# Kernel tuning notes

Hardware: AMD Instinct MI355X
Metric: run time of the kernel (lower is better)

## Reference

```python
import jax, jax.numpy as jnp
import numpy as np

N, S, C, E = 32768, 32768, 1024, 16384   # nodes, subgraph-node entries, clusters (=B*P), coarsen edges
F, D, B, P, NC = 64, 64, 16, 64, 10      # feat dim, hidden, graphs, patches per graph, classes


def setup_inputs():
    key = jax.random.key(0)
    ks = list(jax.random.split(key, 24))
    p = lambda k, shp: jax.random.normal(k, shp, dtype=jnp.float32) * 0.05
    z = lambda n: jnp.zeros((n,), jnp.float32)
    return {
        "x": jax.random.normal(ks[0], (N, F), dtype=jnp.float32),
        "subgraphs_nodes_mapper": jax.random.randint(ks[1], (S,), 0, N, dtype=jnp.int32),
        "subgraphs_batch": jnp.sort(jax.random.randint(ks[2], (S,), 0, C, dtype=jnp.int32)),
        "subgraphs_batch_row": jax.random.randint(ks[3], (E,), 0, C, dtype=jnp.int32),
        "subgraphs_batch_col": jax.random.randint(ks[4], (E,), 0, C, dtype=jnp.int32),
        "coarsen_edge_attr": jax.random.uniform(ks[5], (E,), dtype=jnp.float32),
        "W_in1": p(ks[6], (F, D)), "b_in1": z(D),
        "W_in2": p(ks[7], (D, D)), "b_in2": z(D),
        "W_pre1": p(ks[8], (D, D)), "b_pre1": z(D),
        "W_pre2": p(ks[9], (D, D)), "b_pre2": z(D),
        "W_post1": p(ks[10], (D, D)), "b_post1": z(D),
        "W_post2": p(ks[11], (D, D)), "b_post2": z(D),
        "W_K": p(ks[12], (D, D)), "b_K": z(D),
        "W_V": p(ks[13], (D, D)), "b_V": z(D),
        "alpha_beta": jax.random.normal(ks[14], (2,), dtype=jnp.float32),
        "W_c1": p(ks[15], (D, D // 2)), "b_c1": z(D // 2),
        "W_c2": p(ks[16], (D // 2, NC)), "b_c2": z(NC),
    }


def reference(x, subgraphs_nodes_mapper, subgraphs_batch, subgraphs_batch_row,
              subgraphs_batch_col, coarsen_edge_attr,
              W_in1, b_in1, W_in2, b_in2, W_pre1, b_pre1, W_pre2, b_pre2,
              W_post1, b_post1, W_post2, b_post2, W_K, b_K, W_V, b_V,
              alpha_beta, W_c1, b_c1, W_c2, b_c2):
    seg_sum = lambda v, idx: jax.ops.segment_sum(v, idx, num_segments=C)
    # input transform MLP (use_gnn=False path)
    h = jax.nn.relu(x @ W_in1 + b_in1)
    h = jax.nn.relu(h @ W_in2 + b_in2)
    sx = h[subgraphs_nodes_mapper]                        # [S, D] irregular gather
    b = subgraphs_batch
    row, col = subgraphs_batch_row, subgraphs_batch_col
    # bincount-based symmetric degree normalization of coarsened edge weights
    deg = seg_sum(coarsen_edge_attr, row)                 # [C]
    dinv = jnp.where(deg > 0, deg ** -0.5, 0.0)
    ea = dinv[row] * coarsen_edge_attr * dinv[col]        # [E]
    # Q path: pre-deepset -> scatter sum -> post-deepset
    Q = jax.nn.relu(sx @ W_pre1 + b_pre1) @ W_pre2 + b_pre2
    Qs = seg_sum(Q, b)
    Qs = jax.nn.relu(Qs @ W_post1 + b_post1) @ W_post2 + b_post2  # [C, D]
    # K / V paths
    K = sx @ W_K + b_K                                    # [S, D]
    cnt = jnp.maximum(seg_sum(jnp.ones((S,), sx.dtype), b), 1.0)
    Ks = seg_sum(K, b) / cnt[:, None]                     # scatter-mean [C, D]
    V = sx @ W_V + b_V                                    # [S, D]
    # relu kernelization
    Qk, Kk, Ksk = jax.nn.relu(Qs), jax.nn.relu(K), jax.nn.relu(Ks)
    ab = jax.nn.softmax(alpha_beta)
    sa, sb = ab[0] ** -0.5, ab[1] ** -0.5
    ck = jnp.concatenate([sa * Ksk[b], sb * Kk], axis=-1)   # [S, 2D]
    cq = jnp.concatenate([sa * Qk, sb * Qk], axis=-1)       # [C, 2D] (diffQ=False)
    ck_s = seg_sum(ck, b)                                   # [C, 2D]
    M = ck[:, :, None] * V[:, None, :]                      # [S, 2D, D] per-entry outer product
    Ms = seg_sum(M, b)                                      # [C, 2D, D]
    # Double_Level_MessageProp / KeyProp on coarsened graph: out[c] = sum_e ea_e * x[row_e] at col_e
    Ms = seg_sum(ea[:, None, None] * Ms[row], col)
    ck_s = seg_sum(ea[:, None] * ck_s[row], col)
    H = jnp.einsum('ci,cij->cj', cq, Ms)                    # [C, D]
    den = jnp.sum(cq * ck_s, axis=-1, keepdims=True) + 1e-6
    out = H / den                                           # [C, D]
    g = out.reshape(B, P, D).mean(axis=1)                   # mean readout over patches
    logits = jax.nn.relu(g @ W_c1 + b_c1) @ W_c2 + b_c2     # [B, NC]
    return logits
```

## Files before the change

kernel.cpp:

```cpp
#include <hip/hip_runtime.h>
#include <math.h>

constexpr int NN = 32768;
constexpr int SS = 32768;
constexpr int CC = 1024;
constexpr int EE = 16384;
constexpr int BB = 16;
constexpr int PP = 64;
constexpr int NC = 10;

__device__ __forceinline__ float rdlane(float v, int l) {
    return __int_as_float(__builtin_amdgcn_readlane(__float_as_int(v), l));
}

#define TS 68

__device__ __forceinline__ void gemm64(const float* A, const float* W,
                                       const float* __restrict__ bias,
                                       int r0, int c0, float acc[4][4])
{
#pragma unroll
    for (int dc = 0; dc < 4; ++dc) {
        float bv = bias[c0 + dc];
        acc[0][dc] = bv; acc[1][dc] = bv; acc[2][dc] = bv; acc[3][dc] = bv;
    }
#pragma unroll 16
    for (int k = 0; k < 64; ++k) {
        float4 av = *(const float4*)(A + k * TS + r0);
        float4 wv = *(const float4*)(W + k * TS + c0);
        acc[0][0] = fmaf(av.x, wv.x, acc[0][0]); acc[0][1] = fmaf(av.x, wv.y, acc[0][1]);
        acc[0][2] = fmaf(av.x, wv.z, acc[0][2]); acc[0][3] = fmaf(av.x, wv.w, acc[0][3]);
        acc[1][0] = fmaf(av.y, wv.x, acc[1][0]); acc[1][1] = fmaf(av.y, wv.y, acc[1][1]);
        acc[1][2] = fmaf(av.y, wv.z, acc[1][2]); acc[1][3] = fmaf(av.y, wv.w, acc[1][3]);
        acc[2][0] = fmaf(av.z, wv.x, acc[2][0]); acc[2][1] = fmaf(av.z, wv.y, acc[2][1]);
        acc[2][2] = fmaf(av.z, wv.z, acc[2][2]); acc[2][3] = fmaf(av.z, wv.w, acc[2][3]);
        acc[3][0] = fmaf(av.w, wv.x, acc[3][0]); acc[3][1] = fmaf(av.w, wv.y, acc[3][1]);
        acc[3][2] = fmaf(av.w, wv.z, acc[3][2]); acc[3][3] = fmaf(av.w, wv.w, acc[3][3]);
    }
}

__device__ __forceinline__ void gemm64x2(const float* A, const float* Wa, const float* Wb,
                                         const float* __restrict__ bias1,
                                         const float* __restrict__ bias2,
                                         int r0, int c0, float acc1[4][4], float acc2[4][4])
{
#pragma unroll
    for (int dc = 0; dc < 4; ++dc) {
        float bv1 = bias1[c0 + dc], bv2 = bias2[c0 + dc];
#pragma unroll
        for (int dr = 0; dr < 4; ++dr) { acc1[dr][dc] = bv1; acc2[dr][dc] = bv2; }
    }
#pragma unroll 8
    for (int k = 0; k < 64; ++k) {
        float4 av = *(const float4*)(A + k * TS + r0);
        float4 w1 = *(const float4*)(Wa + k * TS + c0);
        float4 w2 = *(const float4*)(Wb + k * TS + c0);
        float ar[4] = {av.x, av.y, av.z, av.w};
        float u1[4] = {w1.x, w1.y, w1.z, w1.w};
        float u2[4] = {w2.x, w2.y, w2.z, w2.w};
#pragma unroll
        for (int dr = 0; dr < 4; ++dr)
#pragma unroll
            for (int dc = 0; dc < 4; ++dc) {
                acc1[dr][dc] = fmaf(ar[dr], u1[dc], acc1[dr][dc]);
                acc2[dr][dc] = fmaf(ar[dr], u2[dc], acc2[dr][dc]);
            }
    }
}

__device__ __forceinline__ void writeW(float* dst, int tid,
                                       float4 a, float4 b, float4 c, float4 d)
{
    int colq = (tid & 15) * 4;
    int rb = tid >> 4;
    *(float4*)(dst + (rb     ) * TS + colq) = a;
    *(float4*)(dst + (rb + 16) * TS + colq) = b;
    *(float4*)(dst + (rb + 32) * TS + colq) = c;
    *(float4*)(dst + (rb + 48) * TS + colq) = d;
}

__device__ __forceinline__ void writeXT(float* dst, int tid,
                                        float4 a, float4 b, float4 c, float4 d)
{
    int rb = (tid * 4) & 63;
    int cb = tid >> 4;
    dst[(rb + 0) * TS + cb     ] = a.x;
    dst[(rb + 1) * TS + cb     ] = a.y;
    dst[(rb + 2) * TS + cb     ] = a.z;
    dst[(rb + 3) * TS + cb     ] = a.w;
    dst[(rb + 0) * TS + cb + 16] = b.x;
    dst[(rb + 1) * TS + cb + 16] = b.y;
    dst[(rb + 2) * TS + cb + 16] = b.z;
    dst[(rb + 3) * TS + cb + 16] = b.w;
    dst[(rb + 0) * TS + cb + 32] = c.x;
    dst[(rb + 1) * TS + cb + 32] = c.y;
    dst[(rb + 2) * TS + cb + 32] = c.z;
    dst[(rb + 3) * TS + cb + 32] = c.w;
    dst[(rb + 0) * TS + cb + 48] = d.x;
    dst[(rb + 1) * TS + cb + 48] = d.y;
    dst[(rb + 2) * TS + cb + 48] = d.z;
    dst[(rb + 3) * TS + cb + 48] = d.w;
}

__device__ __forceinline__ void outT_relu(float* dst, int r0, int c0, float acc[4][4])
{
#pragma unroll
    for (int dc = 0; dc < 4; ++dc) {
        *(float4*)(dst + (c0 + dc) * TS + r0) =
            make_float4(fmaxf(acc[0][dc], 0.f), fmaxf(acc[1][dc], 0.f),
                        fmaxf(acc[2][dc], 0.f), fmaxf(acc[3][dc], 0.f));
    }
}

__device__ __forceinline__ void outG2(float* __restrict__ dst, size_t rowbase, int ld,
                                      int off, int r0, int c0, float acc[4][4], bool dorelu)
{
#pragma unroll
    for (int dr = 0; dr < 4; ++dr) {
        float4 v = make_float4(acc[dr][0], acc[dr][1], acc[dr][2], acc[dr][3]);
        if (dorelu) {
            v.x = fmaxf(v.x, 0.f); v.y = fmaxf(v.y, 0.f);
            v.z = fmaxf(v.z, 0.f); v.w = fmaxf(v.w, 0.f);
        }
        *(float4*)(dst + (rowbase + r0 + dr) * ld + off + c0) = v;
    }
}

__global__ __launch_bounds__(256, 3) void k_node(
    const float* __restrict__ x,
    const int* __restrict__ row, const float* __restrict__ attr,
    const int* __restrict__ batch,
    const float* __restrict__ W1, const float* __restrict__ b1,
    const float* __restrict__ W2, const float* __restrict__ b2,
    const float* __restrict__ Wp1, const float* __restrict__ bp1,
    const float* __restrict__ WK, const float* __restrict__ bK,
    const float* __restrict__ WV, const float* __restrict__ bV,
    float* __restrict__ u, float* __restrict__ KV,
    float* __restrict__ deg, int* __restrict__ segoff, float* __restrict__ zbase)
{
    __shared__ __align__(16) float bufA[64 * TS];
    __shared__ __align__(16) float bufB[64 * TS];
    __shared__ __align__(16) float w0[64 * TS];
    __shared__ float ldeg[16];
    int tid = threadIdx.x;
    int b = blockIdx.x;
    if (tid < 33) {
        int i = b * 33 + tid;
        if (i < 16640) ((float4*)zbase)[i] = make_float4(0.f, 0.f, 0.f, 0.f);
    }
    if (b < 64) {
        if (tid < 16) ldeg[tid] = 0.f;
        __syncthreads();
        int lo = b * 16;
#pragma unroll 4
        for (int i = 0; i < 64; ++i) {
            int e = i * 256 + tid;
            int r = row[e];
            unsigned d = (unsigned)(r - lo);
            if (d < 16u) atomicAdd(&ldeg[d], attr[e]);
        }
        __syncthreads();
        if (tid < 16) deg[lo + tid] = ldeg[tid];
    } else if (b < 192) {
        int t = (b - 64) * 256 + tid;
        int cur = batch[t];
        int prev = (t == 0) ? -1 : batch[t - 1];
        for (int c = prev + 1; c <= cur; ++c) segoff[c] = t;
        if (t == SS - 1)
            for (int c = cur + 1; c <= CC; ++c) segoff[c] = SS;
    }
    int tx = tid & 15, ty = tid >> 4;
    int r0 = ty * 4, c0 = tx * 4;
    size_t rowbase = (size_t)b * 64;
    const float* xb = x + rowbase * 64;
    float4 a0 = ((const float4*)W1)[tid];
    float4 a1 = ((const float4*)W1)[tid + 256];
    float4 a2 = ((const float4*)W1)[tid + 512];
    float4 a3 = ((const float4*)W1)[tid + 768];
    float4 x0 = ((const float4*)xb)[tid];
    float4 x1 = ((const float4*)xb)[tid + 256];
    float4 x2 = ((const float4*)xb)[tid + 512];
    float4 x3 = ((const float4*)xb)[tid + 768];
    writeW(w0, tid, a0, a1, a2, a3);
    writeXT(bufA, tid, x0, x1, x2, x3);
    __syncthreads();
    float acc[4][4], acc2[4][4];
    a0 = ((const float4*)W2)[tid];
    a1 = ((const float4*)W2)[tid + 256];
    a2 = ((const float4*)W2)[tid + 512];
    a3 = ((const float4*)W2)[tid + 768];
    gemm64(bufA, w0, b1, r0, c0, acc);
    outT_relu(bufB, r0, c0, acc);
    __syncthreads();
    writeW(w0, tid, a0, a1, a2, a3);
    __syncthreads();
    a0 = ((const float4*)Wp1)[tid];
    a1 = ((const float4*)Wp1)[tid + 256];
    a2 = ((const float4*)Wp1)[tid + 512];
    a3 = ((const float4*)Wp1)[tid + 768];
    float4 k0 = ((const float4*)WK)[tid];
    float4 k1 = ((const float4*)WK)[tid + 256];
    float4 k2 = ((const float4*)WK)[tid + 512];
    float4 k3 = ((const float4*)WK)[tid + 768];
    gemm64(bufB, w0, b2, r0, c0, acc);
    outT_relu(bufA, r0, c0, acc);
    __syncthreads();
    writeW(w0, tid, a0, a1, a2, a3);
    writeW(bufB, tid, k0, k1, k2, k3);
    __syncthreads();
    a0 = ((const float4*)WV)[tid];
    a1 = ((const float4*)WV)[tid + 256];
    a2 = ((const float4*)WV)[tid + 512];
    a3 = ((const float4*)WV)[tid + 768];
    gemm64x2(bufA, w0, bufB, bp1, bK, r0, c0, acc, acc2);
    outG2(u, rowbase, 64, 0, r0, c0, acc, true);
    outG2(KV, rowbase, 128, 0, r0, c0, acc2, false);
    __syncthreads();
    writeW(w0, tid, a0, a1, a2, a3);
    __syncthreads();
    gemm64(bufA, w0, bV, r0, c0, acc);
    outG2(KV, rowbase, 128, 64, r0, c0, acc, false);
}

__global__ __launch_bounds__(256, 4) void k_qk(
    const float* __restrict__ u, const int* __restrict__ mapper,
    const int* __restrict__ segoff,
    const float* __restrict__ Wp2, const float* __restrict__ bp2,
    const float* __restrict__ Wpo1, const float* __restrict__ bpo1,
    const float* __restrict__ Wpo2, const float* __restrict__ bpo2,
    float* __restrict__ Qk)
{
    __shared__ float accs[4][64];
    int c = blockIdx.x;
    int tid = threadIdx.x, j = tid & 63, g = tid >> 6;
    int s0 = segoff[c], s1 = segoff[c + 1];
    float L = (float)(s1 - s0);
    if (tid < 64) {
        accs[0][tid] = 0.f;
        accs[1][tid] = L * bp2[tid];
        accs[2][tid] = bpo1[tid];
        accs[3][tid] = bpo2[tid];
    }
    __syncthreads();
    float us = 0.f;
    for (int s = s0 + g; s < s1; s += 4) us += u[(size_t)mapper[s] * 64 + j];
    atomicAdd(&accs[0][j], us);
    __syncthreads();
    float usv = accs[0][j];
    float p = 0.f;
#pragma unroll
    for (int t = 0; t < 16; ++t) {
        int i = g * 16 + t;
        p = fmaf(rdlane(usv, i), Wp2[i * 64 + j], p);
    }
    atomicAdd(&accs[1][j], p);
    __syncthreads();
    float qs = accs[1][j];
    p = 0.f;
#pragma unroll
    for (int t = 0; t < 16; ++t) {
        int i = g * 16 + t;
        p = fmaf(rdlane(qs, i), Wpo1[i * 64 + j], p);
    }
    atomicAdd(&accs[2][j], p);
    __syncthreads();
    float tv = fmaxf(accs[2][j], 0.f);
    p = 0.f;
#pragma unroll
    for (int t = 0; t < 16; ++t) {
        int i = g * 16 + t;
        p = fmaf(rdlane(tv, i), Wpo2[i * 64 + j], p);
    }
    atomicAdd(&accs[3][j], p);
    __syncthreads();
    if (g == 0) Qk[c * 64 + j] = fmaxf(accs[3][j], 0.f);
}

#define KSTR 72
#define MSTR 68

__global__ __launch_bounds__(256, 4) void k_msbedge(
    const float* __restrict__ KV, const int* __restrict__ mapper,
    const int* __restrict__ segoff, const float* __restrict__ Qk,
    const int* __restrict__ row, const int* __restrict__ col,
    const float* __restrict__ attr, const float* __restrict__ deg,
    const float* __restrict__ ab,
    float* __restrict__ H, float* __restrict__ den)
{
    __shared__ __align__(16) float Kr[32 * KSTR];
    __shared__ __align__(16) float Vb[32 * KSTR];
    __shared__ __align__(16) float msb[64 * MSTR];
    __shared__ int map_lds[32];
    __shared__ float sums[192];
    __shared__ float dvec[64];
    __shared__ int eids[128];
    __shared__ int ecol[144];
    __shared__ float ewt[144];
    __shared__ int ecnt;
    int c = blockIdx.x;
    int tid = threadIdx.x, j = tid & 63, g = tid >> 6;
    int tx = tid & 15, ty = tid >> 4;
    int r0 = ty * 4, c0 = tx * 4;
    if (tid == 0) ecnt = 0;
    if (tid < 192) sums[tid] = 0.f;
    __syncthreads();
#pragma unroll 4
    for (int i = 0; i < 64; ++i) {
        int e = i * 256 + tid;
        if (row[e] == c) {
            int p = atomicAdd(&ecnt, 1);
            if (p < 128) eids[p] = e;
        }
    }
    __syncthreads();
    int ne = min(ecnt, 128);
    if (ne == 0) return;
    int s0 = segoff[c], s1 = segoff[c + 1];
    float acc[4][4];
#pragma unroll
    for (int a = 0; a < 4; ++a)
#pragma unroll
        for (int bq = 0; bq < 4; ++bq) acc[a][bq] = 0.f;
    float ks = 0.f, krs = 0.f, vs = 0.f;
    for (int sb = s0; sb < s1; sb += 32) {
        int clen = min(32, s1 - sb);
        __syncthreads();
        if (tid < clen) map_lds[tid] = mapper[sb + tid];
        __syncthreads();
        for (int p = tid; p < clen * 32; p += 256) {
            int e = p >> 5, q = p & 31;
            int m = map_lds[e];
            float4 v = *(const float4*)(KV + (size_t)m * 128 + q * 4);
            float* dst = (q < 16) ? &Kr[e * KSTR + q * 4] : &Vb[e * KSTR + (q - 16) * 4];
            *(float4*)dst = v;
        }
        __syncthreads();
#pragma unroll 4
        for (int s = 0; s < clen; ++s) {
            float4 a4 = *(const float4*)(&Kr[s * KSTR + r0]);
            float4 b4 = *(const float4*)(&Vb[s * KSTR + c0]);
            float ar0 = fmaxf(a4.x, 0.f), ar1 = fmaxf(a4.y, 0.f);
            float ar2 = fmaxf(a4.z, 0.f), ar3 = fmaxf(a4.w, 0.f);
            acc[0][0] = fmaf(ar0, b4.x, acc[0][0]); acc[0][1] = fmaf(ar0, b4.y, acc[0][1]);
            acc[0][2] = fmaf(ar0, b4.z, acc[0][2]); acc[0][3] = fmaf(ar0, b4.w, acc[0][3]);
            acc[1][0] = fmaf(ar1, b4.x, acc[1][0]); acc[1][1] = fmaf(ar1, b4.y, acc[1][1]);
            acc[1][2] = fmaf(ar1, b4.z, acc[1][2]); acc[1][3] = fmaf(ar1, b4.w, acc[1][3]);
            acc[2][0] = fmaf(ar2, b4.x, acc[2][0]); acc[2][1] = fmaf(ar2, b4.y, acc[2][1]);
            acc[2][2] = fmaf(ar2, b4.z, acc[2][2]); acc[2][3] = fmaf(ar2, b4.w, acc[2][3]);
            acc[3][0] = fmaf(ar3, b4.x, acc[3][0]); acc[3][1] = fmaf(ar3, b4.y, acc[3][1]);
            acc[3][2] = fmaf(ar3, b4.z, acc[3][2]); acc[3][3] = fmaf(ar3, b4.w, acc[3][3]);
        }
        for (int s = g; s < clen; s += 4) {
            float kv = Kr[s * KSTR + j];
            ks += kv;
            krs += fmaxf(kv, 0.f);
            vs += Vb[s * KSTR + j];
        }
    }
    atomicAdd(&sums[j], ks);
    atomicAdd(&sums[64 + j], krs);
    atomicAdd(&sums[128 + j], vs);
    __syncthreads();
    int L = s1 - s0;
    float Lr = (float)L;
    float invLm = 1.f / (float)(L > 0 ? L : 1);
    float a0 = ab[0], a1 = ab[1];
    float sa2 = 1.f + expf(a1 - a0);
    float sb2 = 1.f + expf(a0 - a1);
    float dr = deg[c];
    float dinvr = dr > 0.f ? 1.f / sqrtf(dr) : 0.f;
    if (tid < 64) {
        float kskv = fmaxf(sums[tid] * invLm, 0.f);
        dvec[tid] = sa2 * Lr * kskv + sb2 * sums[64 + tid];
    }
    float4 vsl4 = *(const float4*)(&sums[128 + c0]);
#pragma unroll
    for (int a = 0; a < 4; ++a) {
        float kska = fmaxf(sums[r0 + a] * invLm, 0.f) * sa2;
        *(float4*)(&msb[(r0 + a) * MSTR + c0]) =
            make_float4(fmaf(kska, vsl4.x, sb2 * acc[a][0]),
                        fmaf(kska, vsl4.y, sb2 * acc[a][1]),
                        fmaf(kska, vsl4.z, sb2 * acc[a][2]),
                        fmaf(kska, vsl4.w, sb2 * acc[a][3]));
    }
    int nr = (ne + 15) & ~15;
    if (tid < ne) {
        int e = eids[tid];
        int cd = col[e];
        float dc = deg[cd];
        float dinvc = dc > 0.f ? 1.f / sqrtf(dc) : 0.f;
        ecol[tid] = cd;
        ewt[tid] = dinvr * attr[e] * dinvc;
    }
    for (int p = ne + tid; p < nr; p += 256) { ecol[p] = c; ewt[p] = 0.f; }
    __syncthreads();
    float dvreg = dvec[j];
    for (int m0 = g * 4; m0 < nr; m0 += 16) {
        int cd0 = ecol[m0 + 0], cd1 = ecol[m0 + 1];
        int cd2 = ecol[m0 + 2], cd3 = ecol[m0 + 3];
        float wt0 = ewt[m0 + 0], wt1 = ewt[m0 + 1];
        float wt2 = ewt[m0 + 2], wt3 = ewt[m0 + 3];
        float q0 = Qk[(size_t)cd0 * 64 + j];
        float q1 = Qk[(size_t)cd1 * 64 + j];
        float q2 = Qk[(size_t)cd2 * 64 + j];
        float q3 = Qk[(size_t)cd3 * 64 + j];
        float o0 = 0.f, o1 = 0.f, o2 = 0.f, o3 = 0.f;
#pragma unroll
        for (int i = 0; i < 64; ++i) {
            float mv = msb[i * MSTR + j];
            o0 = fmaf(rdlane(q0, i), mv, o0);
            o1 = fmaf(rdlane(q1, i), mv, o1);
            o2 = fmaf(rdlane(q2, i), mv, o2);
            o3 = fmaf(rdlane(q3, i), mv, o3);
        }
        float p0 = q0 * dvreg, p1 = q1 * dvreg, p2 = q2 * dvreg, p3 = q3 * dvreg;
#pragma unroll
        for (int o = 32; o > 0; o >>= 1) {
            p0 += __shfl_xor(p0, o);
            p1 += __shfl_xor(p1, o);
            p2 += __shfl_xor(p2, o);
            p3 += __shfl_xor(p3, o);
        }
        atomicAdd(&H[(size_t)cd0 * 64 + j], wt0 * o0);
        atomicAdd(&H[(size_t)cd1 * 64 + j], wt1 * o1);
        atomicAdd(&H[(size_t)cd2 * 64 + j], wt2 * o2);
        atomicAdd(&H[(size_t)cd3 * 64 + j], wt3 * o3);
        if (j == 0) {
            atomicAdd(&den[cd0], wt0 * p0);
            atomicAdd(&den[cd1], wt1 * p1);
            atomicAdd(&den[cd2], wt2 * p2);
            atomicAdd(&den[cd3], wt3 * p3);
        }
    }
}

__global__ __launch_bounds__(64) void k_final(
    const float* __restrict__ H, const float* __restrict__ den,
    const float* __restrict__ Wc1, const float* __restrict__ bc1,
    const float* __restrict__ Wc2, const float* __restrict__ bc2,
    float* __restrict__ out)
{
    int bg = blockIdx.x;
    int j = threadIdx.x;
    float acc = 0.f;
    for (int p = 0; p < PP; ++p) {
        int c = bg * PP + p;
        acc += H[c * 64 + j] / (den[c] + 1e-6f);
    }
    float g = acc * (1.f / (float)PP);
    int m = j & 31;
    float a1 = bc1[m];
#pragma unroll
    for (int i = 0; i < 64; ++i) a1 = fmaf(rdlane(g, i), Wc1[i * 32 + m], a1);
    float c1 = fmaxf(a1, 0.f);
    int n = (j < NC) ? j : 0;
    float a2 = bc2[n];
#pragma unroll
    for (int i = 0; i < 32; ++i) a2 = fmaf(rdlane(c1, i), Wc2[i * NC + n], a2);
    if (j < NC) out[bg * NC + j] = a2;
}

extern "C" void kernel_launch(void* const* d_in, const int* in_sizes, int n_in,
                              void* d_out, int out_size, void* d_ws, size_t ws_size,
                              hipStream_t stream)
{
    const float* x      = (const float*)d_in[0];
    const int*   mapper = (const int*)d_in[1];
    const int*   batch  = (const int*)d_in[2];
    const int*   row    = (const int*)d_in[3];
    const int*   col    = (const int*)d_in[4];
    const float* attr   = (const float*)d_in[5];
    const float* W_in1  = (const float*)d_in[6];
    const float* b_in1  = (const float*)d_in[7];
    const float* W_in2  = (const float*)d_in[8];
    const float* b_in2  = (const float*)d_in[9];
    const float* W_pre1 = (const float*)d_in[10];
    const float* b_pre1 = (const float*)d_in[11];
    const float* W_pre2 = (const float*)d_in[12];
    const float* b_pre2 = (const float*)d_in[13];
    const float* W_post1= (const float*)d_in[14];
    const float* b_post1= (const float*)d_in[15];
    const float* W_post2= (const float*)d_in[16];
    const float* b_post2= (const float*)d_in[17];
    const float* W_K    = (const float*)d_in[18];
    const float* b_K    = (const float*)d_in[19];
    const float* W_V    = (const float*)d_in[20];
    const float* b_V    = (const float*)d_in[21];
    const float* alpha_beta = (const float*)d_in[22];
    const float* W_c1   = (const float*)d_in[23];
    const float* b_c1   = (const float*)d_in[24];
    const float* W_c2   = (const float*)d_in[25];
    const float* b_c2   = (const float*)d_in[26];

    float* ws = (float*)d_ws;
    float* u     = ws;
    float* KV    = u     + (size_t)NN * 64;
    float* Qk    = KV    + (size_t)NN * 128;
    float* deg   = Qk    + (size_t)CC * 64;
    float* H     = deg   + (size_t)CC;
    float* den   = H     + (size_t)CC * 64;
    int*  segoff = (int*)(den + (size_t)CC);

    k_node<<<NN / 64, 256, 0, stream>>>(x, row, attr, batch,
                                        W_in1, b_in1, W_in2, b_in2,
                                        W_pre1, b_pre1, W_K, b_K, W_V, b_V,
                                        u, KV, deg, segoff, H);
    k_qk<<<CC, 256, 0, stream>>>(u, mapper, segoff, W_pre2, b_pre2,
                                 W_post1, b_post1, W_post2, b_post2, Qk);
    k_msbedge<<<CC, 256, 0, stream>>>(KV, mapper, segoff, Qk, row, col,
                                      attr, deg, alpha_beta, H, den);
    k_final<<<BB, 64, 0, stream>>>(H, den, W_c1, b_c1, W_c2, b_c2, (float*)d_out);
}
```

Before: 94.71 us.

## Split msbedge into half-row blocks and fuse pre1/K/V GEMMs in k_node

k_msbedge now launches two blocks per cluster, each handling half of the 64 key rows of the outer-product accumulator. This shrinks shared memory and registers per block so more blocks fit per CU (launch bounds go from 4 to 6). The cost is that each block reloads the V rows and redoes the edge scan. k_node adds a fourth shared weight buffer and computes the pre1, K and V projections in one three-way GEMM, removing several barriers. That extra LDS lowers its occupancy target from 3 to 2 blocks.

Measured after the change: 114.3 us. 20.7% more time.

```diff
diff --git a/kernel.cpp b/kernel.cpp
--- a/kernel.cpp
+++ b/kernel.cpp
@@ -39,31 +39,37 @@
     }
 }
 
-__device__ __forceinline__ void gemm64x2(const float* A, const float* Wa, const float* Wb,
-                                         const float* __restrict__ bias1,
-                                         const float* __restrict__ bias2,
-                                         int r0, int c0, float acc1[4][4], float acc2[4][4])
+__device__ __forceinline__ void gemm64x3(const float* A, const float* Wa,
+                                         const float* Wb, const float* Wc_,
+                                         const float* __restrict__ b1_,
+                                         const float* __restrict__ b2_,
+                                         const float* __restrict__ b3_,
+                                         int r0, int c0,
+                                         float a1_[4][4], float a2_[4][4], float a3_[4][4])
 {
 #pragma unroll
     for (int dc = 0; dc < 4; ++dc) {
-        float bv1 = bias1[c0 + dc], bv2 = bias2[c0 + dc];
-#pragma unroll
-        for (int dr = 0; dr < 4; ++dr) { acc1[dr][dc] = bv1; acc2[dr][dc] = bv2; }
-    }
-#pragma unroll 8
+        float v1 = b1_[c0 + dc], v2 = b2_[c0 + dc], v3 = b3_[c0 + dc];
+#pragma unroll
+        for (int dr = 0; dr < 4; ++dr) { a1_[dr][dc] = v1; a2_[dr][dc] = v2; a3_[dr][dc] = v3; }
+    }
+#pragma unroll 4
     for (int k = 0; k < 64; ++k) {
         float4 av = *(const float4*)(A + k * TS + r0);
         float4 w1 = *(const float4*)(Wa + k * TS + c0);
         float4 w2 = *(const float4*)(Wb + k * TS + c0);
+        float4 w3 = *(const float4*)(Wc_ + k * TS + c0);
         float ar[4] = {av.x, av.y, av.z, av.w};
         float u1[4] = {w1.x, w1.y, w1.z, w1.w};
         float u2[4] = {w2.x, w2.y, w2.z, w2.w};
+        float u3[4] = {w3.x, w3.y, w3.z, w3.w};
 #pragma unroll
         for (int dr = 0; dr < 4; ++dr)
 #pragma unroll
             for (int dc = 0; dc < 4; ++dc) {
-                acc1[dr][dc] = fmaf(ar[dr], u1[dc], acc1[dr][dc]);
-                acc2[dr][dc] = fmaf(ar[dr], u2[dc], acc2[dr][dc]);
+                a1_[dr][dc] = fmaf(ar[dr], u1[dc], a1_[dr][dc]);
+                a2_[dr][dc] = fmaf(ar[dr], u2[dc], a2_[dr][dc]);
+                a3_[dr][dc] = fmaf(ar[dr], u3[dc], a3_[dr][dc]);
             }
     }
 }
@@ -126,7 +132,7 @@
     }
 }
 
-__global__ __launch_bounds__(256, 3) void k_node(
+__global__ __launch_bounds__(256, 2) void k_node(
     const float* __restrict__ x,
     const int* __restrict__ row, const float* __restrict__ attr,
     const int* __restrict__ batch,
@@ -141,6 +147,7 @@
     __shared__ __align__(16) float bufA[64 * TS];
     __shared__ __align__(16) float bufB[64 * TS];
     __shared__ __align__(16) float w0[64 * TS];
+    __shared__ __align__(16) float w1[64 * TS];
     __shared__ float ldeg[16];
     int tid = threadIdx.x;
     int b = blockIdx.x;
@@ -184,15 +191,14 @@
     writeW(w0, tid, a0, a1, a2, a3);
     writeXT(bufA, tid, x0, x1, x2, x3);
     __syncthreads();
-    float acc[4][4], acc2[4][4];
+    float acc[4][4];
     a0 = ((const float4*)W2)[tid];
     a1 = ((const float4*)W2)[tid + 256];
     a2 = ((const float4*)W2)[tid + 512];
     a3 = ((const float4*)W2)[tid + 768];
     gemm64(bufA, w0, b1, r0, c0, acc);
     outT_relu(bufB, r0, c0, acc);
-    __syncthreads();
-    writeW(w0, tid, a0, a1, a2, a3);
+    writeW(w1, tid, a0, a1, a2, a3);
     __syncthreads();
     a0 = ((const float4*)Wp1)[tid];
     a1 = ((const float4*)Wp1)[tid + 256];
@@ -202,24 +208,21 @@
     float4 k1 = ((const float4*)WK)[tid + 256];
     float4 k2 = ((const float4*)WK)[tid + 512];
     float4 k3 = ((const float4*)WK)[tid + 768];
-    gemm64(bufB, w0, b2, r0, c0, acc);
+    float4 v0 = ((const float4*)WV)[tid];
+    float4 v1 = ((const float4*)WV)[tid + 256];
+    float4 v2 = ((const float4*)WV)[tid + 512];
+    float4 v3 = ((const float4*)WV)[tid + 768];
+    gemm64(bufB, w1, b2, r0, c0, acc);
     outT_relu(bufA, r0, c0, acc);
-    __syncthreads();
     writeW(w0, tid, a0, a1, a2, a3);
-    writeW(bufB, tid, k0, k1, k2, k3);
-    __syncthreads();
-    a0 = ((const float4*)WV)[tid];
-    a1 = ((const float4*)WV)[tid + 256];
-    a2 = ((const float4*)WV)[tid + 512];
-    a3 = ((const float4*)WV)[tid + 768];
-    gemm64x2(bufA, w0, bufB, bp1, bK, r0, c0, acc, acc2);
-    outG2(u, rowbase, 64, 0, r0, c0, acc, true);
-    outG2(KV, rowbase, 128, 0, r0, c0, acc2, false);
-    __syncthreads();
-    writeW(w0, tid, a0, a1, a2, a3);
-    __syncthreads();
-    gemm64(bufA, w0, bV, r0, c0, acc);
-    outG2(KV, rowbase, 128, 64, r0, c0, acc, false);
+    writeW(w1, tid, k0, k1, k2, k3);
+    writeW(bufB, tid, v0, v1, v2, v3);
+    __syncthreads();
+    float accU[4][4], accK[4][4], accV[4][4];
+    gemm64x3(bufA, w0, w1, bufB, bp1, bK, bV, r0, c0, accU, accK, accV);
+    outG2(u, rowbase, 64, 0, r0, c0, accU, true);
+    outG2(KV, rowbase, 128, 0, r0, c0, accK, false);
+    outG2(KV, rowbase, 128, 64, r0, c0, accV, false);
 }
 
 __global__ __launch_bounds__(256, 4) void k_qk(
@@ -276,10 +279,11 @@
     if (g == 0) Qk[c * 64 + j] = fmaxf(accs[3][j], 0.f);
 }
 
-#define KSTR 72
-#define MSTR 68
-
-__global__ __launch_bounds__(256, 4) void k_msbedge(
+#define KS 36
+#define VS 72
+#define MS 68
+
+__global__ __launch_bounds__(256, 6) void k_msbedge(
     const float* __restrict__ KV, const int* __restrict__ mapper,
     const int* __restrict__ segoff, const float* __restrict__ Qk,
     const int* __restrict__ row, const int* __restrict__ col,
@@ -287,22 +291,24 @@
     const float* __restrict__ ab,
     float* __restrict__ H, float* __restrict__ den)
 {
-    __shared__ __align__(16) float Kr[32 * KSTR];
-    __shared__ __align__(16) float Vb[32 * KSTR];
-    __shared__ __align__(16) float msb[64 * MSTR];
+    __shared__ __align__(16) float pool[32 * KS + 32 * VS];
     __shared__ int map_lds[32];
-    __shared__ float sums[192];
-    __shared__ float dvec[64];
+    __shared__ float ksum[32], krsl[32], vsum[64], dvec[32];
     __shared__ int eids[128];
     __shared__ int ecol[144];
     __shared__ float ewt[144];
     __shared__ int ecnt;
-    int c = blockIdx.x;
+    float* Kr  = pool;
+    float* Vb  = pool + 32 * KS;
+    float* msb = pool;
+    int bid = blockIdx.x;
+    int c = bid >> 1, half = bid & 1;
     int tid = threadIdx.x, j = tid & 63, g = tid >> 6;
-    int tx = tid & 15, ty = tid >> 4;
-    int r0 = ty * 4, c0 = tx * 4;
+    int tr = tid >> 4, tc = tid & 15;
+    int i0 = tr * 2, c0 = tc * 4;
     if (tid == 0) ecnt = 0;
-    if (tid < 192) sums[tid] = 0.f;
+    if (tid < 32) { ksum[tid] = 0.f; krsl[tid] = 0.f; }
+    if (tid < 64) vsum[tid] = 0.f;
     __syncthreads();
 #pragma unroll 4
     for (int i = 0; i < 64; ++i) {
@@ -316,50 +322,46 @@
     int ne = min(ecnt, 128);
     if (ne == 0) return;
     int s0 = segoff[c], s1 = segoff[c + 1];
-    float acc[4][4];
-#pragma unroll
-    for (int a = 0; a < 4; ++a)
-#pragma unroll
-        for (int bq = 0; bq < 4; ++bq) acc[a][bq] = 0.f;
+    int koff = half * 32;
+    float acc[2][4] = {{0.f, 0.f, 0.f, 0.f}, {0.f, 0.f, 0.f, 0.f}};
     float ks = 0.f, krs = 0.f, vs = 0.f;
     for (int sb = s0; sb < s1; sb += 32) {
         int clen = min(32, s1 - sb);
         __syncthreads();
         if (tid < clen) map_lds[tid] = mapper[sb + tid];
         __syncthreads();
-        for (int p = tid; p < clen * 32; p += 256) {
-            int e = p >> 5, q = p & 31;
-            int m = map_lds[e];
-            float4 v = *(const float4*)(KV + (size_t)m * 128 + q * 4);
-            float* dst = (q < 16) ? &Kr[e * KSTR + q * 4] : &Vb[e * KSTR + (q - 16) * 4];
-            *(float4*)dst = v;
+        for (int p = tid; p < clen * 8; p += 256) {
+            int e = p >> 3, q = p & 7;
+            *(float4*)(&Kr[e * KS + q * 4]) =
+                *(const float4*)(KV + (size_t)map_lds[e] * 128 + koff + q * 4);
+        }
+        for (int p = tid; p < clen * 16; p += 256) {
+            int e = p >> 4, q = p & 15;
+            *(float4*)(&Vb[e * VS + q * 4]) =
+                *(const float4*)(KV + (size_t)map_lds[e] * 128 + 64 + q * 4);
         }
         __syncthreads();
 #pragma unroll 4
         for (int s = 0; s < clen; ++s) {
-            float4 a4 = *(const float4*)(&Kr[s * KSTR + r0]);
-            float4 b4 = *(const float4*)(&Vb[s * KSTR + c0]);
-            float ar0 = fmaxf(a4.x, 0.f), ar1 = fmaxf(a4.y, 0.f);
-            float ar2 = fmaxf(a4.z, 0.f), ar3 = fmaxf(a4.w, 0.f);
+            float2 a2 = *(const float2*)(&Kr[s * KS + i0]);
+            float4 b4 = *(const float4*)(&Vb[s * VS + c0]);
+            float ar0 = fmaxf(a2.x, 0.f), ar1 = fmaxf(a2.y, 0.f);
             acc[0][0] = fmaf(ar0, b4.x, acc[0][0]); acc[0][1] = fmaf(ar0, b4.y, acc[0][1]);
             acc[0][2] = fmaf(ar0, b4.z, acc[0][2]); acc[0][3] = fmaf(ar0, b4.w, acc[0][3]);
             acc[1][0] = fmaf(ar1, b4.x, acc[1][0]); acc[1][1] = fmaf(ar1, b4.y, acc[1][1]);
             acc[1][2] = fmaf(ar1, b4.z, acc[1][2]); acc[1][3] = fmaf(ar1, b4.w, acc[1][3]);
-            acc[2][0] = fmaf(ar2, b4.x, acc[2][0]); acc[2][1] = fmaf(ar2, b4.y, acc[2][1]);
-            acc[2][2] = fmaf(ar2, b4.z, acc[2][2]); acc[2][3] = fmaf(ar2, b4.w, acc[2][3]);
-            acc[3][0] = fmaf(ar3, b4.x, acc[3][0]); acc[3][1] = fmaf(ar3, b4.y, acc[3][1]);
-            acc[3][2] = fmaf(ar3, b4.z, acc[3][2]); acc[3][3] = fmaf(ar3, b4.w, acc[3][3]);
         }
         for (int s = g; s < clen; s += 4) {
-            float kv = Kr[s * KSTR + j];
-            ks += kv;
-            krs += fmaxf(kv, 0.f);
-            vs += Vb[s * KSTR + j];
-        }
-    }
-    atomicAdd(&sums[j], ks);
-    atomicAdd(&sums[64 + j], krs);
-    atomicAdd(&sums[128 + j], vs);
+            if (j < 32) {
+                float kv = Kr[s * KS + j];
+                ks += kv;
+                krs += fmaxf(kv, 0.f);
+            }
+            vs += Vb[s * VS + j];
+        }
+    }
+    if (j < 32) { atomicAdd(&ksum[j], ks); atomicAdd(&krsl[j], krs); }
+    atomicAdd(&vsum[j], vs);
     __syncthreads();
     int L = s1 - s0;
     float Lr = (float)L;
@@ -369,20 +371,23 @@
     float sb2 = 1.f + expf(a0 - a1);
     float dr = deg[c];
     float dinvr = dr > 0.f ? 1.f / sqrtf(dr) : 0.f;
-    if (tid < 64) {
-        float kskv = fmaxf(sums[tid] * invLm, 0.f);
-        dvec[tid] = sa2 * Lr * kskv + sb2 * sums[64 + tid];
-    }
-    float4 vsl4 = *(const float4*)(&sums[128 + c0]);
-#pragma unroll
-    for (int a = 0; a < 4; ++a) {
-        float kska = fmaxf(sums[r0 + a] * invLm, 0.f) * sa2;
-        *(float4*)(&msb[(r0 + a) * MSTR + c0]) =
-            make_float4(fmaf(kska, vsl4.x, sb2 * acc[a][0]),
-                        fmaf(kska, vsl4.y, sb2 * acc[a][1]),
-                        fmaf(kska, vsl4.z, sb2 * acc[a][2]),
-                        fmaf(kska, vsl4.w, sb2 * acc[a][3]));
-    }
+    {
+        float4 vsl4 = *(const float4*)(&vsum[c0]);
+        float kk0 = fmaxf(ksum[i0] * invLm, 0.f) * sa2;
+        float kk1 = fmaxf(ksum[i0 + 1] * invLm, 0.f) * sa2;
+        *(float4*)(&msb[i0 * MS + c0]) =
+            make_float4(fmaf(kk0, vsl4.x, sb2 * acc[0][0]),
+                        fmaf(kk0, vsl4.y, sb2 * acc[0][1]),
+                        fmaf(kk0, vsl4.z, sb2 * acc[0][2]),
+                        fmaf(kk0, vsl4.w, sb2 * acc[0][3]));
+        *(float4*)(&msb[(i0 + 1) * MS + c0]) =
+            make_float4(fmaf(kk1, vsl4.x, sb2 * acc[1][0]),
+                        fmaf(kk1, vsl4.y, sb2 * acc[1][1]),
+                        fmaf(kk1, vsl4.z, sb2 * acc[1][2]),
+                        fmaf(kk1, vsl4.w, sb2 * acc[1][3]));
+    }
+    if (tid < 32)
+        dvec[tid] = sa2 * Lr * fmaxf(ksum[tid] * invLm, 0.f) + sb2 * krsl[tid];
     int nr = (ne + 15) & ~15;
     if (tid < ne) {
         int e = eids[tid];
@@ -394,26 +399,27 @@
     }
     for (int p = ne + tid; p < nr; p += 256) { ecol[p] = c; ewt[p] = 0.f; }
     __syncthreads();
-    float dvreg = dvec[j];
+    float dvj = (j < 32) ? dvec[j] : 0.f;
+    int jq = half * 32 + (j & 31);
     for (int m0 = g * 4; m0 < nr; m0 += 16) {
         int cd0 = ecol[m0 + 0], cd1 = ecol[m0 + 1];
         int cd2 = ecol[m0 + 2], cd3 = ecol[m0 + 3];
         float wt0 = ewt[m0 + 0], wt1 = ewt[m0 + 1];
         float wt2 = ewt[m0 + 2], wt3 = ewt[m0 + 3];
-        float q0 = Qk[(size_t)cd0 * 64 + j];
-        float q1 = Qk[(size_t)cd1 * 64 + j];
-        float q2 = Qk[(size_t)cd2 * 64 + j];
-        float q3 = Qk[(size_t)cd3 * 64 + j];
+        float q0 = Qk[(size_t)cd0 * 64 + jq];
+        float q1 = Qk[(size_t)cd1 * 64 + jq];
+        float q2 = Qk[(size_t)cd2 * 64 + jq];
+        float q3 = Qk[(size_t)cd3 * 64 + jq];
         float o0 = 0.f, o1 = 0.f, o2 = 0.f, o3 = 0.f;
 #pragma unroll
-        for (int i = 0; i < 64; ++i) {
-            float mv = msb[i * MSTR + j];
+        for (int i = 0; i < 32; ++i) {
+            float mv = msb[i * MS + j];
             o0 = fmaf(rdlane(q0, i), mv, o0);
             o1 = fmaf(rdlane(q1, i), mv, o1);
             o2 = fmaf(rdlane(q2, i), mv, o2);
             o3 = fmaf(rdlane(q3, i), mv, o3);
         }
-        float p0 = q0 * dvreg, p1 = q1 * dvreg, p2 = q2 * dvreg, p3 = q3 * dvreg;
+        float p0 = q0 * dvj, p1 = q1 * dvj, p2 = q2 * dvj, p3 = q3 * dvj;
 #pragma unroll
         for (int o = 32; o > 0; o >>= 1) {
             p0 += __shfl_xor(p0, o);
@@ -507,7 +513,7 @@
                                         u, KV, deg, segoff, H);
     k_qk<<<CC, 256, 0, stream>>>(u, mapper, segoff, W_pre2, b_pre2,
                                  W_post1, b_post1, W_post2, b_post2, Qk);
-    k_msbedge<<<CC, 256, 0, stream>>>(KV, mapper, segoff, Qk, row, col,
-                                      attr, deg, alpha_beta, H, den);
+    k_msbedge<<<2 * CC, 256, 0, stream>>>(KV, mapper, segoff, Qk, row, col,
+                                          attr, deg, alpha_beta, H, den);
     k_final<<<BB, 64, 0, stream>>>(H, den, W_c1, b_c1, W_c2, b_c2, (float*)d_out);
 }
```

## Prebucket edges by row in node kernel and fuse Wpre1/K/V GEMMs

Applied to the files above, without the earlier changes.

Edge scanning by source row moves out of k_msbedge, where each of 1024 blocks scanned all 16384 edges. 256 extra blocks in k_node now build per-cluster edge buckets capped at 64 entries, and k_msbedge reads these precomputed lists. k_node also fuses the three final 64x64 GEMMs (pre1, K, V) into one pass using a fourth shared-memory weight buffer, which removes several barriers. The extra LDS lowers the occupancy target from 3 to 2 blocks, and the lower edge cap (64 vs 128) could drop edges if any cluster has a larger out-degree.

Result: faster. 89.94 us (-5.0%).

```diff
diff --git a/kernel.cpp b/kernel.cpp
--- a/kernel.cpp
+++ b/kernel.cpp
@@ -8,6 +8,7 @@
 constexpr int BB = 16;
 constexpr int PP = 64;
 constexpr int NC = 10;
+constexpr int ECAP = 64;
 
 __device__ __forceinline__ float rdlane(float v, int l) {
     return __int_as_float(__builtin_amdgcn_readlane(__float_as_int(v), l));
@@ -39,31 +40,37 @@
     }
 }
 
-__device__ __forceinline__ void gemm64x2(const float* A, const float* Wa, const float* Wb,
-                                         const float* __restrict__ bias1,
-                                         const float* __restrict__ bias2,
-                                         int r0, int c0, float acc1[4][4], float acc2[4][4])
+__device__ __forceinline__ void gemm64x3(const float* A, const float* Wa,
+                                         const float* Wb, const float* Wc_,
+                                         const float* __restrict__ b1_,
+                                         const float* __restrict__ b2_,
+                                         const float* __restrict__ b3_,
+                                         int r0, int c0,
+                                         float a1_[4][4], float a2_[4][4], float a3_[4][4])
 {
 #pragma unroll
     for (int dc = 0; dc < 4; ++dc) {
-        float bv1 = bias1[c0 + dc], bv2 = bias2[c0 + dc];
-#pragma unroll
-        for (int dr = 0; dr < 4; ++dr) { acc1[dr][dc] = bv1; acc2[dr][dc] = bv2; }
-    }
-#pragma unroll 8
+        float v1 = b1_[c0 + dc], v2 = b2_[c0 + dc], v3 = b3_[c0 + dc];
+#pragma unroll
+        for (int dr = 0; dr < 4; ++dr) { a1_[dr][dc] = v1; a2_[dr][dc] = v2; a3_[dr][dc] = v3; }
+    }
+#pragma unroll 4
     for (int k = 0; k < 64; ++k) {
         float4 av = *(const float4*)(A + k * TS + r0);
         float4 w1 = *(const float4*)(Wa + k * TS + c0);
         float4 w2 = *(const float4*)(Wb + k * TS + c0);
+        float4 w3 = *(const float4*)(Wc_ + k * TS + c0);
         float ar[4] = {av.x, av.y, av.z, av.w};
         float u1[4] = {w1.x, w1.y, w1.z, w1.w};
         float u2[4] = {w2.x, w2.y, w2.z, w2.w};
+        float u3[4] = {w3.x, w3.y, w3.z, w3.w};
 #pragma unroll
         for (int dr = 0; dr < 4; ++dr)
 #pragma unroll
             for (int dc = 0; dc < 4; ++dc) {
-                acc1[dr][dc] = fmaf(ar[dr], u1[dc], acc1[dr][dc]);
-                acc2[dr][dc] = fmaf(ar[dr], u2[dc], acc2[dr][dc]);
+                a1_[dr][dc] = fmaf(ar[dr], u1[dc], a1_[dr][dc]);
+                a2_[dr][dc] = fmaf(ar[dr], u2[dc], a2_[dr][dc]);
+                a3_[dr][dc] = fmaf(ar[dr], u3[dc], a3_[dr][dc]);
             }
     }
 }
@@ -126,7 +133,7 @@
     }
 }
 
-__global__ __launch_bounds__(256, 3) void k_node(
+__global__ __launch_bounds__(256, 2) void k_node(
     const float* __restrict__ x,
     const int* __restrict__ row, const float* __restrict__ attr,
     const int* __restrict__ batch,
@@ -136,12 +143,16 @@
     const float* __restrict__ WK, const float* __restrict__ bK,
     const float* __restrict__ WV, const float* __restrict__ bV,
     float* __restrict__ u, float* __restrict__ KV,
-    float* __restrict__ deg, int* __restrict__ segoff, float* __restrict__ zbase)
+    float* __restrict__ deg, int* __restrict__ segoff,
+    int* __restrict__ gcnt, int* __restrict__ ebuck,
+    float* __restrict__ zbase)
 {
     __shared__ __align__(16) float bufA[64 * TS];
     __shared__ __align__(16) float bufB[64 * TS];
     __shared__ __align__(16) float w0[64 * TS];
+    __shared__ __align__(16) float w1[64 * TS];
     __shared__ float ldeg[16];
+    __shared__ int lbk[4];
     int tid = threadIdx.x;
     int b = blockIdx.x;
     if (tid < 33) {
@@ -168,6 +179,22 @@
         for (int c = prev + 1; c <= cur; ++c) segoff[c] = t;
         if (t == SS - 1)
             for (int c = cur + 1; c <= CC; ++c) segoff[c] = SS;
+    } else if (b < 448) {
+        int crow = (b - 192) * 4;
+        if (tid < 4) lbk[tid] = 0;
+        __syncthreads();
+#pragma unroll 4
+        for (int i = 0; i < 64; ++i) {
+            int e = i * 256 + tid;
+            int r = row[e];
+            unsigned d = (unsigned)(r - crow);
+            if (d < 4u) {
+                int pos = atomicAdd(&lbk[d], 1);
+                if (pos < ECAP) ebuck[(size_t)(crow + d) * ECAP + pos] = e;
+            }
+        }
+        __syncthreads();
+        if (tid < 4) gcnt[crow + tid] = min(lbk[tid], ECAP);
     }
     int tx = tid & 15, ty = tid >> 4;
     int r0 = ty * 4, c0 = tx * 4;
@@ -184,15 +211,14 @@
     writeW(w0, tid, a0, a1, a2, a3);
     writeXT(bufA, tid, x0, x1, x2, x3);
     __syncthreads();
-    float acc[4][4], acc2[4][4];
+    float acc[4][4];
     a0 = ((const float4*)W2)[tid];
     a1 = ((const float4*)W2)[tid + 256];
     a2 = ((const float4*)W2)[tid + 512];
     a3 = ((const float4*)W2)[tid + 768];
     gemm64(bufA, w0, b1, r0, c0, acc);
     outT_relu(bufB, r0, c0, acc);
-    __syncthreads();
-    writeW(w0, tid, a0, a1, a2, a3);
+    writeW(w1, tid, a0, a1, a2, a3);
     __syncthreads();
     a0 = ((const float4*)Wp1)[tid];
     a1 = ((const float4*)Wp1)[tid + 256];
@@ -202,24 +228,21 @@
     float4 k1 = ((const float4*)WK)[tid + 256];
     float4 k2 = ((const float4*)WK)[tid + 512];
     float4 k3 = ((const float4*)WK)[tid + 768];
-    gemm64(bufB, w0, b2, r0, c0, acc);
+    float4 v0 = ((const float4*)WV)[tid];
+    float4 v1 = ((const float4*)WV)[tid + 256];
+    float4 v2 = ((const float4*)WV)[tid + 512];
+    float4 v3 = ((const float4*)WV)[tid + 768];
+    gemm64(bufB, w1, b2, r0, c0, acc);
     outT_relu(bufA, r0, c0, acc);
-    __syncthreads();
     writeW(w0, tid, a0, a1, a2, a3);
-    writeW(bufB, tid, k0, k1, k2, k3);
-    __syncthreads();
-    a0 = ((const float4*)WV)[tid];
-    a1 = ((const float4*)WV)[tid + 256];
-    a2 = ((const float4*)WV)[tid + 512];
-    a3 = ((const float4*)WV)[tid + 768];
-    gemm64x2(bufA, w0, bufB, bp1, bK, r0, c0, acc, acc2);
-    outG2(u, rowbase, 64, 0, r0, c0, acc, true);
-    outG2(KV, rowbase, 128, 0, r0, c0, acc2, false);
-    __syncthreads();
-    writeW(w0, tid, a0, a1, a2, a3);
-    __syncthreads();
-    gemm64(bufA, w0, bV, r0, c0, acc);
-    outG2(KV, rowbase, 128, 64, r0, c0, acc, false);
+    writeW(w1, tid, k0, k1, k2, k3);
+    writeW(bufB, tid, v0, v1, v2, v3);
+    __syncthreads();
+    float accU[4][4], accK[4][4], accV[4][4];
+    gemm64x3(bufA, w0, w1, bufB, bp1, bK, bV, r0, c0, accU, accK, accV);
+    outG2(u, rowbase, 64, 0, r0, c0, accU, true);
+    outG2(KV, rowbase, 128, 0, r0, c0, accK, false);
+    outG2(KV, rowbase, 128, 64, r0, c0, accV, false);
 }
 
 __global__ __launch_bounds__(256, 4) void k_qk(
@@ -282,8 +305,9 @@
 __global__ __launch_bounds__(256, 4) void k_msbedge(
     const float* __restrict__ KV, const int* __restrict__ mapper,
     const int* __restrict__ segoff, const float* __restrict__ Qk,
-    const int* __restrict__ row, const int* __restrict__ col,
-    const float* __restrict__ attr, const float* __restrict__ deg,
+    const int* __restrict__ col, const float* __restrict__ attr,
+    const float* __restrict__ deg,
+    const int* __restrict__ gcnt, const int* __restrict__ ebuck,
     const float* __restrict__ ab,
     float* __restrict__ H, float* __restrict__ den)
 {
@@ -293,28 +317,27 @@
     __shared__ int map_lds[32];
     __shared__ float sums[192];
     __shared__ float dvec[64];
-    __shared__ int eids[128];
-    __shared__ int ecol[144];
-    __shared__ float ewt[144];
-    __shared__ int ecnt;
+    __shared__ int ecol[ECAP];
+    __shared__ float ewt[ECAP];
     int c = blockIdx.x;
     int tid = threadIdx.x, j = tid & 63, g = tid >> 6;
     int tx = tid & 15, ty = tid >> 4;
     int r0 = ty * 4, c0 = tx * 4;
-    if (tid == 0) ecnt = 0;
+    int ne = gcnt[c];
+    if (ne == 0) return;
+    int nr = (ne + 15) & ~15;
     if (tid < 192) sums[tid] = 0.f;
-    __syncthreads();
-#pragma unroll 4
-    for (int i = 0; i < 64; ++i) {
-        int e = i * 256 + tid;
-        if (row[e] == c) {
-            int p = atomicAdd(&ecnt, 1);
-            if (p < 128) eids[p] = e;
-        }
-    }
-    __syncthreads();
-    int ne = min(ecnt, 128);
-    if (ne == 0) return;
+    if (tid < ne) {
+        int e = ebuck[(size_t)c * ECAP + tid];
+        int cd = col[e];
+        float dc = deg[cd];
+        float dinvc = dc > 0.f ? 1.f / sqrtf(dc) : 0.f;
+        float drr = deg[c];
+        float dinvr = drr > 0.f ? 1.f / sqrtf(drr) : 0.f;
+        ecol[tid] = cd;
+        ewt[tid] = dinvr * attr[e] * dinvc;
+    }
+    for (int p = ne + tid; p < nr; p += 256) { ecol[p] = c; ewt[p] = 0.f; }
     int s0 = segoff[c], s1 = segoff[c + 1];
     float acc[4][4];
 #pragma unroll
@@ -367,8 +390,6 @@
     float a0 = ab[0], a1 = ab[1];
     float sa2 = 1.f + expf(a1 - a0);
     float sb2 = 1.f + expf(a0 - a1);
-    float dr = deg[c];
-    float dinvr = dr > 0.f ? 1.f / sqrtf(dr) : 0.f;
     if (tid < 64) {
         float kskv = fmaxf(sums[tid] * invLm, 0.f);
         dvec[tid] = sa2 * Lr * kskv + sb2 * sums[64 + tid];
@@ -383,16 +404,6 @@
                         fmaf(kska, vsl4.z, sb2 * acc[a][2]),
                         fmaf(kska, vsl4.w, sb2 * acc[a][3]));
     }
-    int nr = (ne + 15) & ~15;
-    if (tid < ne) {
-        int e = eids[tid];
-        int cd = col[e];
-        float dc = deg[cd];
-        float dinvc = dc > 0.f ? 1.f / sqrtf(dc) : 0.f;
-        ecol[tid] = cd;
-        ewt[tid] = dinvr * attr[e] * dinvc;
-    }
-    for (int p = ne + tid; p < nr; p += 256) { ecol[p] = c; ewt[p] = 0.f; }
     __syncthreads();
     float dvreg = dvec[j];
     for (int m0 = g * 4; m0 < nr; m0 += 16) {
@@ -500,14 +511,16 @@
     float* H     = deg   + (size_t)CC;
     float* den   = H     + (size_t)CC * 64;
     int*  segoff = (int*)(den + (size_t)CC);
+    int*  gcnt   = segoff + (CC + 1);
+    int*  ebuck  = gcnt + CC;
 
     k_node<<<NN / 64, 256, 0, stream>>>(x, row, attr, batch,
                                         W_in1, b_in1, W_in2, b_in2,
                                         W_pre1, b_pre1, W_K, b_K, W_V, b_V,
-                                        u, KV, deg, segoff, H);
+                                        u, KV, deg, segoff, gcnt, ebuck, H);
     k_qk<<<CC, 256, 0, stream>>>(u, mapper, segoff, W_pre2, b_pre2,
                                  W_post1, b_post1, W_post2, b_post2, Qk);
-    k_msbedge<<<CC, 256, 0, stream>>>(KV, mapper, segoff, Qk, row, col,
-                                      attr, deg, alpha_beta, H, den);
+    k_msbedge<<<CC, 256, 0, stream>>>(KV, mapper, segoff, Qk, col, attr,
+                                      deg, gcnt, ebuck, alpha_beta, H, den);
     k_final<<<BB, 64, 0, stream>>>(H, den, W_c1, b_c1, W_c2, b_c2, (float*)d_out);
 }
```

## Prebucket coarsen edges by row in node kernel; software-pipeline gathers

Applied to the files above, without the earlier changes.

Moves the per-cluster scan over all 16384 edges out of k_msbedge. It is replaced by a bucketing pass run in spare blocks of k_node, which writes per-row edge lists capped at 64 entries and their counts. k_msbedge then reads only its own bucket and computes the edge weights up front. Separately, the segment gather in k_qk and the edge loop in k_msbedge are software-pipelined to prefetch the next iteration's loads. The cap shrinks from 128 to 64 edges per row, which could drop edges for high-degree rows, and the bucketing adds work to k_node.

New measurement: 95.26 us. Within noise of the previous version (+0.6%).

```diff
diff --git a/kernel.cpp b/kernel.cpp
--- a/kernel.cpp
+++ b/kernel.cpp
@@ -8,6 +8,7 @@
 constexpr int BB = 16;
 constexpr int PP = 64;
 constexpr int NC = 10;
+constexpr int ECAP = 64;
 
 __device__ __forceinline__ float rdlane(float v, int l) {
     return __int_as_float(__builtin_amdgcn_readlane(__float_as_int(v), l));
@@ -136,12 +137,15 @@
     const float* __restrict__ WK, const float* __restrict__ bK,
     const float* __restrict__ WV, const float* __restrict__ bV,
     float* __restrict__ u, float* __restrict__ KV,
-    float* __restrict__ deg, int* __restrict__ segoff, float* __restrict__ zbase)
+    float* __restrict__ deg, int* __restrict__ segoff,
+    int* __restrict__ gcnt, int* __restrict__ ebuck,
+    float* __restrict__ zbase)
 {
     __shared__ __align__(16) float bufA[64 * TS];
     __shared__ __align__(16) float bufB[64 * TS];
     __shared__ __align__(16) float w0[64 * TS];
     __shared__ float ldeg[16];
+    __shared__ int lbk[4];
     int tid = threadIdx.x;
     int b = blockIdx.x;
     if (tid < 33) {
@@ -168,6 +172,22 @@
         for (int c = prev + 1; c <= cur; ++c) segoff[c] = t;
         if (t == SS - 1)
             for (int c = cur + 1; c <= CC; ++c) segoff[c] = SS;
+    } else if (b < 448) {
+        int crow = (b - 192) * 4;
+        if (tid < 4) lbk[tid] = 0;
+        __syncthreads();
+#pragma unroll 4
+        for (int i = 0; i < 64; ++i) {
+            int e = i * 256 + tid;
+            int r = row[e];
+            unsigned d = (unsigned)(r - crow);
+            if (d < 4u) {
+                int pos = atomicAdd(&lbk[d], 1);
+                if (pos < ECAP) ebuck[(size_t)(crow + d) * ECAP + pos] = e;
+            }
+        }
+        __syncthreads();
+        if (tid < 4) gcnt[crow + tid] = min(lbk[tid], ECAP);
     }
     int tx = tid & 15, ty = tid >> 4;
     int r0 = ty * 4, c0 = tx * 4;
@@ -243,7 +263,21 @@
     }
     __syncthreads();
     float us = 0.f;
-    for (int s = s0 + g; s < s1; s += 4) us += u[(size_t)mapper[s] * 64 + j];
+    {
+        int s = s0 + g;
+        if (s < s1) {
+            float uv = u[(size_t)mapper[s] * 64 + j];
+            for (;;) {
+                int s2 = s + 4;
+                float uv2 = 0.f;
+                if (s2 < s1) uv2 = u[(size_t)mapper[s2] * 64 + j];
+                us += uv;
+                if (s2 >= s1) break;
+                uv = uv2;
+                s = s2;
+            }
+        }
+    }
     atomicAdd(&accs[0][j], us);
     __syncthreads();
     float usv = accs[0][j];
@@ -282,8 +316,9 @@
 __global__ __launch_bounds__(256, 4) void k_msbedge(
     const float* __restrict__ KV, const int* __restrict__ mapper,
     const int* __restrict__ segoff, const float* __restrict__ Qk,
-    const int* __restrict__ row, const int* __restrict__ col,
-    const float* __restrict__ attr, const float* __restrict__ deg,
+    const int* __restrict__ col, const float* __restrict__ attr,
+    const float* __restrict__ deg,
+    const int* __restrict__ gcnt, const int* __restrict__ ebuck,
     const float* __restrict__ ab,
     float* __restrict__ H, float* __restrict__ den)
 {
@@ -293,28 +328,27 @@
     __shared__ int map_lds[32];
     __shared__ float sums[192];
     __shared__ float dvec[64];
-    __shared__ int eids[128];
-    __shared__ int ecol[144];
-    __shared__ float ewt[144];
-    __shared__ int ecnt;
+    __shared__ int ecol[ECAP];
+    __shared__ float ewt[ECAP];
     int c = blockIdx.x;
     int tid = threadIdx.x, j = tid & 63, g = tid >> 6;
     int tx = tid & 15, ty = tid >> 4;
     int r0 = ty * 4, c0 = tx * 4;
-    if (tid == 0) ecnt = 0;
+    int ne = gcnt[c];
+    if (ne == 0) return;
+    int nr = (ne + 15) & ~15;
     if (tid < 192) sums[tid] = 0.f;
-    __syncthreads();
-#pragma unroll 4
-    for (int i = 0; i < 64; ++i) {
-        int e = i * 256 + tid;
-        if (row[e] == c) {
-            int p = atomicAdd(&ecnt, 1);
-            if (p < 128) eids[p] = e;
-        }
-    }
-    __syncthreads();
-    int ne = min(ecnt, 128);
-    if (ne == 0) return;
+    if (tid < ne) {
+        int e = ebuck[(size_t)c * ECAP + tid];
+        int cd = col[e];
+        float dc = deg[cd];
+        float dinvc = dc > 0.f ? 1.f / sqrtf(dc) : 0.f;
+        float drr = deg[c];
+        float dinvr = drr > 0.f ? 1.f / sqrtf(drr) : 0.f;
+        ecol[tid] = cd;
+        ewt[tid] = dinvr * attr[e] * dinvc;
+    }
+    for (int p = ne + tid; p < nr; p += 256) { ecol[p] = c; ewt[p] = 0.f; }
     int s0 = segoff[c], s1 = segoff[c + 1];
     float acc[4][4];
 #pragma unroll
@@ -367,8 +401,6 @@
     float a0 = ab[0], a1 = ab[1];
     float sa2 = 1.f + expf(a1 - a0);
     float sb2 = 1.f + expf(a0 - a1);
-    float dr = deg[c];
-    float dinvr = dr > 0.f ? 1.f / sqrtf(dr) : 0.f;
     if (tid < 64) {
         float kskv = fmaxf(sums[tid] * invLm, 0.f);
         dvec[tid] = sa2 * Lr * kskv + sb2 * sums[64 + tid];
@@ -383,27 +415,33 @@
                         fmaf(kska, vsl4.z, sb2 * acc[a][2]),
                         fmaf(kska, vsl4.w, sb2 * acc[a][3]));
     }
-    int nr = (ne + 15) & ~15;
-    if (tid < ne) {
-        int e = eids[tid];
-        int cd = col[e];
-        float dc = deg[cd];
-        float dinvc = dc > 0.f ? 1.f / sqrtf(dc) : 0.f;
-        ecol[tid] = cd;
-        ewt[tid] = dinvr * attr[e] * dinvc;
-    }
-    for (int p = ne + tid; p < nr; p += 256) { ecol[p] = c; ewt[p] = 0.f; }
     __syncthreads();
     float dvreg = dvec[j];
-    for (int m0 = g * 4; m0 < nr; m0 += 16) {
-        int cd0 = ecol[m0 + 0], cd1 = ecol[m0 + 1];
-        int cd2 = ecol[m0 + 2], cd3 = ecol[m0 + 3];
-        float wt0 = ewt[m0 + 0], wt1 = ewt[m0 + 1];
-        float wt2 = ewt[m0 + 2], wt3 = ewt[m0 + 3];
-        float q0 = Qk[(size_t)cd0 * 64 + j];
-        float q1 = Qk[(size_t)cd1 * 64 + j];
-        float q2 = Qk[(size_t)cd2 * 64 + j];
-        float q3 = Qk[(size_t)cd3 * 64 + j];
+    int m0 = g * 4;
+    if (m0 >= nr) return;
+    int cd0 = ecol[m0 + 0], cd1 = ecol[m0 + 1];
+    int cd2 = ecol[m0 + 2], cd3 = ecol[m0 + 3];
+    float wt0 = ewt[m0 + 0], wt1 = ewt[m0 + 1];
+    float wt2 = ewt[m0 + 2], wt3 = ewt[m0 + 3];
+    float q0 = Qk[(size_t)cd0 * 64 + j];
+    float q1 = Qk[(size_t)cd1 * 64 + j];
+    float q2 = Qk[(size_t)cd2 * 64 + j];
+    float q3 = Qk[(size_t)cd3 * 64 + j];
+    for (; m0 < nr; ) {
+        int n0 = m0 + 16;
+        int ncd0 = 0, ncd1 = 0, ncd2 = 0, ncd3 = 0;
+        float nwt0 = 0.f, nwt1 = 0.f, nwt2 = 0.f, nwt3 = 0.f;
+        float nq0 = 0.f, nq1 = 0.f, nq2 = 0.f, nq3 = 0.f;
+        if (n0 < nr) {
+            ncd0 = ecol[n0 + 0]; ncd1 = ecol[n0 + 1];
+            ncd2 = ecol[n0 + 2]; ncd3 = ecol[n0 + 3];
+            nwt0 = ewt[n0 + 0]; nwt1 = ewt[n0 + 1];
+            nwt2 = ewt[n0 + 2]; nwt3 = ewt[n0 + 3];
+            nq0 = Qk[(size_t)ncd0 * 64 + j];
+            nq1 = Qk[(size_t)ncd1 * 64 + j];
+            nq2 = Qk[(size_t)ncd2 * 64 + j];
+            nq3 = Qk[(size_t)ncd3 * 64 + j];
+        }
         float o0 = 0.f, o1 = 0.f, o2 = 0.f, o3 = 0.f;
 #pragma unroll
         for (int i = 0; i < 64; ++i) {
@@ -431,6 +469,10 @@
             atomicAdd(&den[cd2], wt2 * p2);
             atomicAdd(&den[cd3], wt3 * p3);
         }
+        m0 = n0;
+        cd0 = ncd0; cd1 = ncd1; cd2 = ncd2; cd3 = ncd3;
+        wt0 = nwt0; wt1 = nwt1; wt2 = nwt2; wt3 = nwt3;
+        q0 = nq0; q1 = nq1; q2 = nq2; q3 = nq3;
     }
 }
 
@@ -500,14 +542,16 @@
     float* H     = deg   + (size_t)CC;
     float* den   = H     + (size_t)CC * 64;
     int*  segoff = (int*)(den + (size_t)CC);
+    int*  gcnt   = segoff + (CC + 1);
+    int*  ebuck  = gcnt + CC;
 
     k_node<<<NN / 64, 256, 0, stream>>>(x, row, attr, batch,
                                         W_in1, b_in1, W_in2, b_in2,
                                         W_pre1, b_pre1, W_K, b_K, W_V, b_V,
-                                        u, KV, deg, segoff, H);
+                                        u, KV, deg, segoff, gcnt, ebuck, H);
     k_qk<<<CC, 256, 0, stream>>>(u, mapper, segoff, W_pre2, b_pre2,
                                  W_post1, b_post1, W_post2, b_post2, Qk);
-    k_msbedge<<<CC, 256, 0, stream>>>(KV, mapper, segoff, Qk, row, col,
-                                      attr, deg, alpha_beta, H, den);
+    k_msbedge<<<CC, 256, 0, stream>>>(KV, mapper, segoff, Qk, col, attr,
+                                      deg, gcnt, ebuck, alpha_beta, H, den);
     k_final<<<BB, 64, 0, stream>>>(H, den, W_c1, b_c1, W_c2, b_c2, (float*)d_out);
 }
```
